# Kernel tuning notes

Hardware: AMD Instinct MI355X
Metric: run time of the kernel (lower is better)

Reference implementation:

```python
import jax, jax.numpy as jnp
import numpy as np

EPS_LOG = 1e-08   # module eps (added inside log)
EPS_PD = 1e-06    # torch.nn.PairwiseDistance default eps (added to the difference)


def setup_inputs() -> dict:
    key = jax.random.key(0)
    x = jax.random.normal(key, (8192, 512), dtype=jnp.float32)
    return {"x": x}


def reference(x) -> jnp.ndarray:
    n = x.shape[0]
    # Cosine/dot similarity matrix [n, n]; mask the diagonal with -1 so a
    # point cannot be its own nearest neighbor.
    dots = x @ x.T
    idx = jnp.arange(n)
    dots = dots.at[idx, idx].set(-1.0)
    # Nearest neighbor (by dot product) per row; indices — no gradient path.
    I = jnp.argmax(dots, axis=1)
    # PairwiseDistance(p=2): ||x - x[I] + eps||_2 per row.
    diff = x - x[I] + EPS_PD
    rho = jnp.sqrt(jnp.sum(diff * diff, axis=1))
    loss = -jnp.mean(jnp.log(rho + EPS_LOG))
    return loss
```

## Files before the change

kernel.cpp:

```cpp
#include <hip/hip_runtime.h>


#define NPTS 8192
#define DIM  512
#define BM   128
#define BN   128
#define NTIL 64
#define NBLK (NTIL * (NTIL + 1) / 2)
#define KT_N 8

typedef float f32x16 __attribute__((ext_vector_type(16)));
typedef int   i32x4  __attribute__((ext_vector_type(4)));
typedef int   i32x8  __attribute__((ext_vector_type(8)));

__device__ __forceinline__ unsigned char f32_to_e4m3(float f) {
  unsigned u = __builtin_bit_cast(unsigned, f);
  unsigned s = (u >> 24) & 0x80u;
  unsigned a = u & 0x7FFFFFFFu;
  float af = __builtin_bit_cast(float, a);
  if (af < 0.015625f) {
    int m = (int)rintf(af * 512.0f);
    return (unsigned char)(s | (unsigned)m);
  }
  unsigned u2 = a + 0x0007FFFFu + ((a >> 20) & 1u);
  int e = (int)(u2 >> 23) - 127 + 7;
  unsigned m = (u2 >> 20) & 7u;
  if (e > 15) return (unsigned char)(s | 0x7Eu);
  return (unsigned char)(s | ((unsigned)e << 3) | m);
}

__device__ __forceinline__ unsigned int mono_f32(float f) {
  unsigned u = __builtin_bit_cast(unsigned, f);
  return u ^ (0x80000000u | (unsigned)((int)u >> 31));
}

__global__ void cvt_fp8_kernel(const float* __restrict__ x,
                               unsigned char* __restrict__ xq,
                               unsigned long long* __restrict__ nn64) {
  int i = blockIdx.x * blockDim.x + threadIdx.x;
  const float4* xp = reinterpret_cast<const float4*>(x) + 2 * (size_t)i;
  float4 v0 = xp[0], v1 = xp[1];
  unsigned long long w =
      (unsigned long long)f32_to_e4m3(v0.x) |
      ((unsigned long long)f32_to_e4m3(v0.y) << 8) |
      ((unsigned long long)f32_to_e4m3(v0.z) << 16) |
      ((unsigned long long)f32_to_e4m3(v0.w) << 24) |
      ((unsigned long long)f32_to_e4m3(v1.x) << 32) |
      ((unsigned long long)f32_to_e4m3(v1.y) << 40) |
      ((unsigned long long)f32_to_e4m3(v1.z) << 48) |
      ((unsigned long long)f32_to_e4m3(v1.w) << 56);
  reinterpret_cast<unsigned long long*>(xq)[i] = w;
  if (i < NPTS) nn64[i] = 0ull;
}

__device__ __forceinline__ void gload_lds16(const unsigned char* g,
                                            unsigned char* l) {
  __builtin_amdgcn_global_load_lds(
      (__attribute__((address_space(1))) const void*)g,
      (__attribute__((address_space(3))) void*)l, 16, 0, 0);
}

__device__ __forceinline__ unsigned long long kmax(unsigned long long a,
                                                   unsigned long long b) {
  return a > b ? a : b;
}

__global__ __launch_bounds__(256, 3) void tri_gemm_kernel(
    const unsigned char* __restrict__ xq,
    unsigned long long* __restrict__ nn64) {
  __shared__ unsigned char lds[3][16384];

  const int orig = (int)blockIdx.x;
  int b = (orig & 7) * (NBLK >> 3) + (orig >> 3);
  int ti = (int)((sqrtf(8.0f * (float)b + 1.0f) - 1.0f) * 0.5f);
  while ((ti + 1) * (ti + 2) / 2 <= b) ++ti;
  while (ti * (ti + 1) / 2 > b) --ti;
  const int tj = b - ti * (ti + 1) / 2;

  const int tid  = (int)threadIdx.x;
  const int wid  = tid >> 6;
  const int lane = tid & 63;
  const int wr   = wid >> 1;
  const int wc   = wid & 1;
  const int l31  = lane & 31;
  const int h    = lane >> 5;
  const int arow0 = ti * BM;
  const int bcol0 = tj * BN;

#define STAGE(bufi, kt) do {                                                 \
    _Pragma("unroll")                                                        \
    for (int i_ = 0; i_ < 2; ++i_) {                                         \
      const int chunk_ = (i_ << 8) + tid;                        \
      const int row_   = chunk_ >> 2;                            \
      const int f_     = ((row_ >> 1) + (row_ >> 3)) & 3;                    \
      const int c_     = ((chunk_ & 3) - f_) & 3;                            \
      gload_lds16(xq + (size_t)(arow0 + row_) * DIM + (kt) * 64 + (c_ << 4), \
                  &lds[bufi][chunk_ << 4]);                                   \
      gload_lds16(xq + (size_t)(bcol0 + row_) * DIM + (kt) * 64 + (c_ << 4), \
                  &lds[bufi][8192 + (chunk_ << 4)]);                          \
    }                                                                        \
  } while (0)

  const int fr  = ((l31 >> 1) + (l31 >> 3)) & 3;
  const int s0  = (2 * h + fr) & 3;
  const int s1  = (2 * h + 1 + fr) & 3;
  const int abase = (wr * 64 + l31) * 64;
  const int bbase = 8192 + (wc * 64 + l31) * 64;
  const int aoff0 = abase + (s0 << 4), aoff1 = abase + (s1 << 4);
  const int boff0 = bbase + (s0 << 4), boff1 = bbase + (s1 << 4);

  f32x16 acc[2][2];
#pragma unroll
  for (int mi = 0; mi < 2; ++mi)
#pragma unroll
    for (int ni = 0; ni < 2; ++ni)
#pragma unroll
      for (int r = 0; r < 16; ++r) acc[mi][ni][r] = 0.f;

  STAGE(0, 0);
  STAGE(1, 1);

  for (int u = 0; u < KT_N; ++u) {
    const int cur = u - (u / 3) * 3;
    if (u == KT_N - 1) {
      asm volatile("s_waitcnt vmcnt(0)" ::: "memory");
    } else {
      asm volatile("s_waitcnt vmcnt(4)" ::: "memory");
    }
    asm volatile("s_barrier" ::: "memory");
    if (u + 2 < KT_N) {
      const int nb = (u + 2) - ((u + 2) / 3) * 3;
      STAGE(nb, u + 2);
    }

    i32x8 a8[2], b8[2];
#pragma unroll
    for (int mi = 0; mi < 2; ++mi) {
      i32x4 lo = *reinterpret_cast<const i32x4*>(&lds[cur][aoff0 + mi * 2048]);
      i32x4 hi = *reinterpret_cast<const i32x4*>(&lds[cur][aoff1 + mi * 2048]);
      a8[mi] = (i32x8){lo[0], lo[1], lo[2], lo[3], hi[0], hi[1], hi[2], hi[3]};
    }
#pragma unroll
    for (int ni = 0; ni < 2; ++ni) {
      i32x4 lo = *reinterpret_cast<const i32x4*>(&lds[cur][boff0 + ni * 2048]);
      i32x4 hi = *reinterpret_cast<const i32x4*>(&lds[cur][boff1 + ni * 2048]);
      b8[ni] = (i32x8){lo[0], lo[1], lo[2], lo[3], hi[0], hi[1], hi[2], hi[3]};
    }
    __builtin_amdgcn_s_setprio(1);
#pragma unroll
    for (int mi = 0; mi < 2; ++mi)
#pragma unroll
      for (int ni = 0; ni < 2; ++ni)
        acc[mi][ni] = __builtin_amdgcn_mfma_scale_f32_32x32x64_f8f6f4(
            a8[mi], b8[ni], acc[mi][ni], 0, 0,
            0, 0x7F7F7F7F, 0, 0x7F7F7F7F);
    __builtin_amdgcn_s_setprio(0);
  }
#undef STAGE

  const bool diagw = (ti == tj) && (wr == wc);

  unsigned long long K[32];
  const unsigned jb = ~(unsigned)(bcol0 + wc * 64 + l31);
#pragma unroll
  for (int mi = 0; mi < 2; ++mi)
#pragma unroll
    for (int r = 0; r < 16; ++r) {
      const int rl = (r & 3) + 8 * (r >> 2) + 4 * h;
      unsigned long long best = 0ull;
#pragma unroll
      for (int ni = 0; ni < 2; ++ni) {
        unsigned long long kk =
            ((unsigned long long)mono_f32(acc[mi][ni][r]) << 32) |
            (unsigned)(jb - ni * 32);
        if (diagw && mi == ni && rl == l31) kk = 0ull;
        best = kmax(best, kk);
      }
      K[mi * 16 + r] = best;
    }
#pragma unroll
  for (int k = 0; k < 5; ++k) {
    const int m = 1 << k;
    const unsigned kb = (unsigned)(lane >> k) & 1u;
#pragma unroll
    for (int i = 0; i < (16 >> k); ++i) {
      unsigned long long lo = K[2 * i], hi = K[2 * i + 1];
      unsigned long long keep = kb ? hi : lo;
      unsigned long long send = kb ? lo : hi;
      unsigned long long recv =
          (unsigned long long)__shfl_xor((long long)send, m);
      K[i] = kmax(keep, recv);
    }
  }
  {
    const int s = l31;
    const int gi = arow0 + wr * 64 + (s >> 4) * 32 +
                   ((s & 3) + 8 * ((s & 15) >> 2) + 4 * h);
    atomicMax(&nn64[gi], K[0]);
  }

  {
    unsigned long long C0 = 0ull, C1 = 0ull;
    const unsigned ib = ~(unsigned)(arow0 + wr * 64);
#pragma unroll
    for (int mi = 0; mi < 2; ++mi)
#pragma unroll
      for (int r = 0; r < 16; ++r) {
        const int rl = (r & 3) + 8 * (r >> 2) + 4 * h;
        const unsigned idxk = (unsigned)(ib - (mi * 32 + rl));
        unsigned long long k0 =
            ((unsigned long long)mono_f32(acc[mi][0][r]) << 32) | idxk;
        if (diagw && mi == 0 && rl == l31) k0 = 0ull;
        C0 = kmax(C0, k0);
        unsigned long long k1 =
            ((unsigned long long)mono_f32(acc[mi][1][r]) << 32) | idxk;
        if (diagw && mi == 1 && rl == l31) k1 = 0ull;
        C1 = kmax(C1, k1);
      }
    unsigned long long keep = h ? C1 : C0;
    unsigned long long send = h ? C0 : C1;
    unsigned long long recv =
        (unsigned long long)__shfl_xor((long long)send, 32);
    unsigned long long R = kmax(keep, recv);
    const int gj = bcol0 + wc * 64 + h * 32 + l31;
    atomicMax(&nn64[gj], R);
  }
}

__global__ void dist_log_kernel(const float* __restrict__ x,
                                const unsigned long long* __restrict__ nn64,
                                float* __restrict__ logs) {
  const int row  = blockIdx.x * 4 + ((int)threadIdx.x >> 6);
  const int lane = (int)threadIdx.x & 63;
  const int nn   = (int)(~(unsigned int)(nn64[row] & 0xFFFFFFFFull)) & (NPTS - 1);
  const float4* xr = reinterpret_cast<const float4*>(x + (size_t)row * DIM);
  const float4* xn = reinterpret_cast<const float4*>(x + (size_t)nn  * DIM);
  float s = 0.f;
#pragma unroll
  for (int i = 0; i < 2; ++i) {
    float4 a = xr[lane + i * 64];
    float4 b = xn[lane + i * 64];
    float d0 = a.x - b.x + 1e-6f;
    float d1 = a.y - b.y + 1e-6f;
    float d2 = a.z - b.z + 1e-6f;
    float d3 = a.w - b.w + 1e-6f;
    s += d0 * d0 + d1 * d1 + d2 * d2 + d3 * d3;
  }
#pragma unroll
  for (int m = 32; m >= 1; m >>= 1) s += __shfl_xor(s, m);
  if (lane == 0) logs[row] = logf(sqrtf(s) + 1e-8f);
}

__global__ void final_reduce_kernel(const float* __restrict__ logs,
                                    float* __restrict__ out) {
  __shared__ float sm[1024];
  const int t = (int)threadIdx.x;
  float s = 0.f;
#pragma unroll
  for (int i = 0; i < 8; ++i) s += logs[t * 8 + i];
  sm[t] = s;
  __syncthreads();
  for (int k = 512; k > 0; k >>= 1) {
    if (t < k) sm[t] += sm[t + k];
    __syncthreads();
  }
  if (t == 0) out[0] = -(sm[0] / (float)NPTS);
}

extern "C" void kernel_launch(void* const* d_in, const int* in_sizes, int n_in,
                              void* d_out, int out_size, void* d_ws, size_t ws_size,
                              hipStream_t stream) {
  const float* x = (const float*)d_in[0];
  float* out = (float*)d_out;
  char* ws = (char*)d_ws;

  unsigned char*      xq   = (unsigned char*)(ws);
  unsigned long long* nn64 = (unsigned long long*)(ws + 4194304);
  float*              logs = (float*)(ws + 4259840);

  cvt_fp8_kernel<<<(NPTS * DIM / 8) / 256, 256, 0, stream>>>(x, xq, nn64);

  tri_gemm_kernel<<<NBLK, 256, 0, stream>>>(xq, nn64);

  dist_log_kernel<<<NPTS / 4, 256, 0, stream>>>(x, nn64, logs);

  final_reduce_kernel<<<1, 1024, 0, stream>>>(logs, out);
}
```

Measured before the change: 50.17 us.

## Load GEMM operands directly from global into registers, dropping LDS staging

Removes the triple-buffered LDS staging (global_load_lds plus barriers) for the fp8 tile GEMM. Each wave now loads its MFMA operand fragments straight from global memory into registers, double-buffered in registers across a fully unrolled K loop. This drops LDS traffic and block-wide barriers, but each operand row is now fetched by both waves that use it, and the loads are strided 16-byte accesses. Register pressure also rises, which may affect occupancy.

```diff
diff --git a/kernel.cpp b/kernel.cpp
--- a/kernel.cpp
+++ b/kernel.cpp
@@ -7,7 +7,6 @@
 #define BN   128
 #define NTIL 64
 #define NBLK (NTIL * (NTIL + 1) / 2)
-#define KT_N 8
 
 typedef float f32x16 __attribute__((ext_vector_type(16)));
 typedef int   i32x4  __attribute__((ext_vector_type(4)));
@@ -53,13 +52,6 @@
   if (i < NPTS) nn64[i] = 0ull;
 }
 
-__device__ __forceinline__ void gload_lds16(const unsigned char* g,
-                                            unsigned char* l) {
-  __builtin_amdgcn_global_load_lds(
-      (__attribute__((address_space(1))) const void*)g,
-      (__attribute__((address_space(3))) void*)l, 16, 0, 0);
-}
-
 __device__ __forceinline__ unsigned long long kmax(unsigned long long a,
                                                    unsigned long long b) {
   return a > b ? a : b;
@@ -68,8 +60,6 @@
 __global__ __launch_bounds__(256, 3) void tri_gemm_kernel(
     const unsigned char* __restrict__ xq,
     unsigned long long* __restrict__ nn64) {
-  __shared__ unsigned char lds[3][16384];
-
   const int orig = (int)blockIdx.x;
   int b = (orig & 7) * (NBLK >> 3) + (orig >> 3);
   int ti = (int)((sqrtf(8.0f * (float)b + 1.0f) - 1.0f) * 0.5f);
@@ -87,76 +77,69 @@
   const int arow0 = ti * BM;
   const int bcol0 = tj * BN;
 
-#define STAGE(bufi, kt) do {                                                 \
-    _Pragma("unroll")                                                        \
-    for (int i_ = 0; i_ < 2; ++i_) {                                         \
-      const int chunk_ = (i_ << 8) + tid;                        \
-      const int row_   = chunk_ >> 2;                            \
-      const int f_     = ((row_ >> 1) + (row_ >> 3)) & 3;                    \
-      const int c_     = ((chunk_ & 3) - f_) & 3;                            \
-      gload_lds16(xq + (size_t)(arow0 + row_) * DIM + (kt) * 64 + (c_ << 4), \
-                  &lds[bufi][chunk_ << 4]);                                   \
-      gload_lds16(xq + (size_t)(bcol0 + row_) * DIM + (kt) * 64 + (c_ << 4), \
-                  &lds[bufi][8192 + (chunk_ << 4)]);                          \
-    }                                                                        \
+  const i32x4* pa0 = reinterpret_cast<const i32x4*>(
+      xq + (size_t)(arow0 + wr * 64 + l31) * DIM + h * 32);
+  const i32x4* pa1 = reinterpret_cast<const i32x4*>(
+      xq + (size_t)(arow0 + wr * 64 + 32 + l31) * DIM + h * 32);
+  const i32x4* pb0 = reinterpret_cast<const i32x4*>(
+      xq + (size_t)(bcol0 + wc * 64 + l31) * DIM + h * 32);
+  const i32x4* pb1 = reinterpret_cast<const i32x4*>(
+      xq + (size_t)(bcol0 + wc * 64 + 32 + l31) * DIM + h * 32);
+
+  f32x16 acc[2][2];
+#pragma unroll
+  for (int mi = 0; mi < 2; ++mi)
+#pragma unroll
+    for (int ni = 0; ni < 2; ++ni)
+#pragma unroll
+      for (int r = 0; r < 16; ++r) acc[mi][ni][r] = 0.f;
+
+#define DECL_SET(S) i32x4 a0l##S, a0h##S, a1l##S, a1h##S,                    \
+                          b0l##S, b0h##S, b1l##S, b1h##S;
+  DECL_SET(0)
+  DECL_SET(1)
+#undef DECL_SET
+
+#define ISSUE(S, kt) do {                                                    \
+    a0l##S = pa0[(kt) * 4];     a0h##S = pa0[(kt) * 4 + 1];                  \
+    a1l##S = pa1[(kt) * 4];     a1h##S = pa1[(kt) * 4 + 1];                  \
+    b0l##S = pb0[(kt) * 4];     b0h##S = pb0[(kt) * 4 + 1];                  \
+    b1l##S = pb1[(kt) * 4];     b1h##S = pb1[(kt) * 4 + 1];                  \
   } while (0)
 
-  const int fr  = ((l31 >> 1) + (l31 >> 3)) & 3;
-  const int s0  = (2 * h + fr) & 3;
-  const int s1  = (2 * h + 1 + fr) & 3;
-  const int abase = (wr * 64 + l31) * 64;
-  const int bbase = 8192 + (wc * 64 + l31) * 64;
-  const int aoff0 = abase + (s0 << 4), aoff1 = abase + (s1 << 4);
-  const int boff0 = bbase + (s0 << 4), boff1 = bbase + (s1 << 4);
-
-  f32x16 acc[2][2];
-#pragma unroll
-  for (int mi = 0; mi < 2; ++mi)
-#pragma unroll
-    for (int ni = 0; ni < 2; ++ni)
-#pragma unroll
-      for (int r = 0; r < 16; ++r) acc[mi][ni][r] = 0.f;
-
-  STAGE(0, 0);
-  STAGE(1, 1);
-
-  for (int u = 0; u < KT_N; ++u) {
-    const int cur = u - (u / 3) * 3;
-    if (u == KT_N - 1) {
-      asm volatile("s_waitcnt vmcnt(0)" ::: "memory");
-    } else {
-      asm volatile("s_waitcnt vmcnt(4)" ::: "memory");
-    }
-    asm volatile("s_barrier" ::: "memory");
-    if (u + 2 < KT_N) {
-      const int nb = (u + 2) - ((u + 2) / 3) * 3;
-      STAGE(nb, u + 2);
-    }
-
-    i32x8 a8[2], b8[2];
-#pragma unroll
-    for (int mi = 0; mi < 2; ++mi) {
-      i32x4 lo = *reinterpret_cast<const i32x4*>(&lds[cur][aoff0 + mi * 2048]);
-      i32x4 hi = *reinterpret_cast<const i32x4*>(&lds[cur][aoff1 + mi * 2048]);
-      a8[mi] = (i32x8){lo[0], lo[1], lo[2], lo[3], hi[0], hi[1], hi[2], hi[3]};
-    }
-#pragma unroll
-    for (int ni = 0; ni < 2; ++ni) {
-      i32x4 lo = *reinterpret_cast<const i32x4*>(&lds[cur][boff0 + ni * 2048]);
-      i32x4 hi = *reinterpret_cast<const i32x4*>(&lds[cur][boff1 + ni * 2048]);
-      b8[ni] = (i32x8){lo[0], lo[1], lo[2], lo[3], hi[0], hi[1], hi[2], hi[3]};
-    }
-    __builtin_amdgcn_s_setprio(1);
-#pragma unroll
-    for (int mi = 0; mi < 2; ++mi)
-#pragma unroll
-      for (int ni = 0; ni < 2; ++ni)
-        acc[mi][ni] = __builtin_amdgcn_mfma_scale_f32_32x32x64_f8f6f4(
-            a8[mi], b8[ni], acc[mi][ni], 0, 0,
-            0, 0x7F7F7F7F, 0, 0x7F7F7F7F);
-    __builtin_amdgcn_s_setprio(0);
-  }
-#undef STAGE
+#define MFMA_T(S) do {                                                       \
+    i32x8 a8_0 = (i32x8){a0l##S[0], a0l##S[1], a0l##S[2], a0l##S[3],         \
+                         a0h##S[0], a0h##S[1], a0h##S[2], a0h##S[3]};        \
+    i32x8 a8_1 = (i32x8){a1l##S[0], a1l##S[1], a1l##S[2], a1l##S[3],         \
+                         a1h##S[0], a1h##S[1], a1h##S[2], a1h##S[3]};        \
+    i32x8 b8_0 = (i32x8){b0l##S[0], b0l##S[1], b0l##S[2], b0l##S[3],         \
+                         b0h##S[0], b0h##S[1], b0h##S[2], b0h##S[3]};        \
+    i32x8 b8_1 = (i32x8){b1l##S[0], b1l##S[1], b1l##S[2], b1l##S[3],         \
+                         b1h##S[0], b1h##S[1], b1h##S[2], b1h##S[3]};        \
+    __builtin_amdgcn_s_setprio(1);                                           \
+    acc[0][0] = __builtin_amdgcn_mfma_scale_f32_32x32x64_f8f6f4(             \
+        a8_0, b8_0, acc[0][0], 0, 0, 0, 0x7F7F7F7F, 0, 0x7F7F7F7F);          \
+    acc[0][1] = __builtin_amdgcn_mfma_scale_f32_32x32x64_f8f6f4(             \
+        a8_0, b8_1, acc[0][1], 0, 0, 0, 0x7F7F7F7F, 0, 0x7F7F7F7F);          \
+    acc[1][0] = __builtin_amdgcn_mfma_scale_f32_32x32x64_f8f6f4(             \
+        a8_1, b8_0, acc[1][0], 0, 0, 0, 0x7F7F7F7F, 0, 0x7F7F7F7F);          \
+    acc[1][1] = __builtin_amdgcn_mfma_scale_f32_32x32x64_f8f6f4(             \
+        a8_1, b8_1, acc[1][1], 0, 0, 0, 0x7F7F7F7F, 0, 0x7F7F7F7F);          \
+    __builtin_amdgcn_s_setprio(0);                                           \
+  } while (0)
+
+  ISSUE(0, 0);
+  ISSUE(1, 1);
+  MFMA_T(0); ISSUE(0, 2);
+  MFMA_T(1); ISSUE(1, 3);
+  MFMA_T(0); ISSUE(0, 4);
+  MFMA_T(1); ISSUE(1, 5);
+  MFMA_T(0); ISSUE(0, 6);
+  MFMA_T(1); ISSUE(1, 7);
+  MFMA_T(0);
+  MFMA_T(1);
+#undef ISSUE
+#undef MFMA_T
 
   const bool diagw = (ti == tj) && (wr == wc);
 
```

After: 86.26 us. +72.0%, slower.
